# Kernel tuning notes

Measured on AMD Instinct MI355X. Metric: run time of the kernel, lower is better.

The kernel has to match this reference:

```python
import jax, jax.numpy as jnp
import numpy as np

B, M, PAST, FUT, NPRED, D = 512, 32768, 8, 12, 20, 48


def _gru_step(h, x, w_ih, w_hh, b_ih, b_hh):
    # torch GRU cell: gates ordered [r, z, n]
    gi = x @ w_ih.T + b_ih
    gh = h @ w_hh.T + b_hh
    ir, iz, inn = jnp.split(gi, 3, axis=-1)
    hr, hz, hn = jnp.split(gh, 3, axis=-1)
    r = jax.nn.sigmoid(ir + hr)
    z = jax.nn.sigmoid(iz + hz)
    n = jnp.tanh(inn + r * hn)
    return (1.0 - z) * n + z * h


def setup_inputs() -> dict:
    key = jax.random.key(0)
    ks = jax.random.split(key, 16)
    f32 = jnp.float32
    def rn(k, shp, sc):
        return (jax.random.normal(k, shp, dtype=f32) * sc)
    return {
        "past": jax.random.normal(ks[0], (B, PAST, 2), dtype=f32),
        "obs_traj": jax.random.normal(ks[1], (B, PAST, 2), dtype=f32),
        "conv_w": rn(ks[2], (D, 2, 3), 0.3),
        "conv_b": jnp.zeros((D,), f32),
        "enc_w_ih": rn(ks[3], (3 * D, D), 0.1),
        "enc_w_hh": rn(ks[4], (3 * D, D), 0.1),
        "enc_b_ih": jnp.zeros((3 * D,), f32),
        "enc_b_hh": jnp.zeros((3 * D,), f32),
        "memory_past": jax.random.normal(ks[5], (M, D), dtype=f32),
        "memory_fut": jax.random.normal(ks[6], (M, D), dtype=f32),
        "Wq": rn(ks[7], (D, D), 0.1), "bq": jnp.zeros((D,), f32),
        "Wk": rn(ks[8], (D, D), 0.1), "bk": jnp.zeros((D,), f32),
        "Wv": rn(ks[9], (D, D), 0.1), "bv": jnp.zeros((D,), f32),
        "dec_w_ih": rn(ks[10], (6 * D, 2 * D), 0.1),
        "dec_w_hh": rn(ks[11], (6 * D, 2 * D), 0.1),
        "dec_b_ih": jnp.zeros((6 * D,), f32),
        "dec_b_hh": jnp.zeros((6 * D,), f32),
        "fc_w": rn(ks[12], (2, 2 * D), 0.1),
        "fc_b": jnp.zeros((2,), f32),
    }


def reference(past, obs_traj, conv_w, conv_b, enc_w_ih, enc_w_hh, enc_b_ih, enc_b_hh,
              memory_past, memory_fut, Wq, bq, Wk, bk, Wv, bv,
              dec_w_ih, dec_w_hh, dec_b_ih, dec_b_hh, fc_w, fc_b):
    b = past.shape[0]
    # --- past encoder: Conv1d(2,48,3,pad=1) + ReLU, then GRU(48,48) ---
    x = jnp.transpose(past, (0, 2, 1))                     # [B,2,T]
    emb = jax.lax.conv_general_dilated(
        x, conv_w, (1,), [(1, 1)], dimension_numbers=("NCH", "OIH", "NCH"))
    emb = jax.nn.relu(emb + conv_b[None, :, None])         # [B,48,T]
    emb = jnp.transpose(emb, (2, 0, 1))                    # [T,B,48] for scan

    def enc_step(h, x_t):
        return _gru_step(h, x_t, enc_w_ih, enc_w_hh, enc_b_ih, enc_b_hh), None
    state_past, _ = jax.lax.scan(enc_step, jnp.zeros((b, D), past.dtype), emb)  # [B,48]

    # --- iterative refinement: 20 rounds of attention over the full memory ---
    # Lin_K/Lin_V are applied to the same (full) banks every iteration -> hoist.
    K = memory_past @ Wk.T + bk                            # [M,48]
    V = memory_fut @ Wv.T + bv                             # [M,48]

    def irm_step(c, _):
        q = c @ Wq.T + bq                                  # [B,48]
        a = jax.nn.softmax(q @ K.T, axis=-1)               # [B,M], scale=1.0
        att = a @ V                                        # [B,48]
        return q + att, att
    _, atts = jax.lax.scan(irm_step, state_past, None, length=NPRED)  # [20,B,48]
    pred = jnp.transpose(atts, (1, 0, 2)).reshape(-1, D)   # [B*20,48] (b-major)

    # --- GRU(96,96) decoder, future_len steps, input only at t=0 ---
    n = b * NPRED
    present = jnp.repeat(obs_traj[:, -1], NPRED, axis=0)   # [B*20,2]
    sp = jnp.repeat(state_past, NPRED, axis=0)             # [B*20,48]
    info = jnp.concatenate([sp, pred], axis=1)             # [B*20,96]
    xs = jnp.concatenate(
        [info[None], jnp.zeros((FUT - 1, n, 2 * D), info.dtype)], axis=0)

    def dec_step(carry, x_t):
        h, pres = carry
        h = _gru_step(h, x_t, dec_w_ih, dec_w_hh, dec_b_ih, dec_b_hh)
        pres = pres + (h @ fc_w.T + fc_b)
        return (h, pres), pres
    _, coords = jax.lax.scan(
        dec_step, (jnp.zeros((n, 2 * D), info.dtype), present), xs)  # [FUT,B*20,2]

    prediction = jnp.transpose(coords, (1, 0, 2)).reshape(b, NPRED, FUT, 2)
    return prediction
```

## Files before the change

### kernel.cpp

```cpp
#include <hip/hip_runtime.h>

typedef unsigned short u16;
typedef unsigned int u32;
typedef __attribute__((ext_vector_type(8))) short short8v;
typedef __attribute__((ext_vector_type(4))) float f32x4;

#define GLD_LDS(g, l) __builtin_amdgcn_global_load_lds( \
    (const __attribute__((address_space(1))) void*)(g), \
    (__attribute__((address_space(3))) void*)(l), 16, 0, 0)

#define LOG2E 1.44269504f

__device__ __forceinline__ u16 f2bf(float f){
  union { float f; u32 u; } v; v.f = f;
  u32 r = v.u + 0x7FFFu + ((v.u >> 16) & 1u);
  return (u16)(r >> 16);
}
__device__ __forceinline__ float bf2f(u16 h){
  union { u32 u; float f; } v; v.u = ((u32)h) << 16;
  return v.f;
}
__device__ __forceinline__ u32 pk2(float a, float b){
  union { float f; u32 u; } x, y; x.f = a; y.f = b;
  return __builtin_amdgcn_perm(y.u + 0x8000u, x.u + 0x8000u, 0x07060302u);
}
__device__ __forceinline__ float sigm(float x){ return 1.f/(1.f+__expf(-x)); }
__device__ __forceinline__ float tanh_fast(float x){ return 1.f - 2.f/(1.f+__expf(2.f*x)); }

__global__ __launch_bounds__(256) void setup_kernel(
    const float* past, const float* conv_w, const float* conv_b,
    const float* enc_w_ih, const float* enc_w_hh, const float* enc_b_ih, const float* enc_b_hh,
    const float* memory_past, const float* memory_fut,
    const float* Wq, const float* bq, const float* Wk, const float* bk,
    const float* Wv, const float* bv,
    const float* dec_w_ih, const float* dec_w_hh,
    float* stateP, float* qf, u16* qbB,
    u16* Kb, u16* Vc, u16* Dihf, u16* Dhhf, u16* WqF)
{
  __shared__ __align__(16) char SMEM[61440];
  const int tid = threadIdx.x, bx = blockIdx.x;
  const int wid = tid>>6, lane = tid&63, qd = lane>>4, ln = lane&15;
  f32x4 zf = {0.f,0.f,0.f,0.f};

  if (tid < 108){
    int which = (tid >= 54) ? 1 : 0;
    int e = bx*54 + (tid - which*54);
    const float* src = which ? dec_w_hh : dec_w_ih;
    u16* dst = which ? Dhhf : Dihf;
    int j = e&7, l2 = (e>>3)&15, q2 = (e>>7)&3, tkc = e>>9;
    int kc = tkc % 3, nt = tkc / 3;
    dst[e] = f2bf(src[(nt*16+l2)*96 + kc*32 + q2*8 + j]);
  }
  if (bx < 12){
    int e = bx*256 + tid;
    int j = e&7, l2 = (e>>3)&15, q2 = (e>>7)&3, tkc = e>>9;
    int kc = tkc&1, nt = tkc>>1;
    int g = nt*16+l2, k = kc*32+q2*8+j;
    WqF[e] = (k < 48) ? f2bf(Wq[g*48+k]) : (u16)0;
  }

  if (bx >= 504){
    int eb = bx - 504;
    u16* sWih = (u16*)(SMEM);
    u16* sWhh = (u16*)(SMEM + 18432);
    u16* sWq  = (u16*)(SMEM + 36864);
    float* sCw = (float*)(SMEM + 43008);
    float* sCb = (float*)(SMEM + 44160);
    float* sPast = (float*)(SMEM + 44352);
    u16* sHbW = (u16*)(SMEM + 48448 + wid*2304);
    for (int e0 = tid; e0 < 21504; e0 += 256){
      int e = e0; const float* src; u16* dst;
      if (e < 9216){ src = enc_w_ih; dst = sWih; }
      else if (e < 18432){ e -= 9216; src = enc_w_hh; dst = sWhh; }
      else { e -= 18432; src = Wq; dst = sWq; }
      int j = e&7, l2 = (e>>3)&15, q2 = (e>>7)&3, tkc = e>>9;
      int kc = tkc&1, nt = tkc>>1;
      int g = nt*16+l2, k = kc*32+q2*8+j;
      dst[e] = (k < 48) ? f2bf(src[g*48+k]) : (u16)0;
    }
    for (int i = tid; i < 288; i += 256) sCw[i] = conv_w[i];
    if (tid < 48) sCb[tid] = conv_b[tid];
    for (int i = tid; i < 1024; i += 256) sPast[i] = past[eb*1024 + i];
    __syncthreads();
    short8v aE[8][2];
    {
      const float* pr = &sPast[(wid*16 + ln)*16];
      for (int t = 0; t < 8; ++t)
        for (int kc = 0; kc < 2; ++kc){
          union { short8v v; u16 h[8]; } u;
          #pragma unroll
          for (int j = 0; j < 8; ++j){
            int d = kc*32 + qd*8 + j;
            float a = 0.f;
            if (d < 48){
              a = sCb[d];
              #pragma unroll
              for (int kt = 0; kt < 3; ++kt){
                int tau = t + kt - 1;
                if (tau >= 0 && tau < 8){
                  a += pr[tau*2+0]*sCw[d*6+kt];
                  a += pr[tau*2+1]*sCw[d*6+3+kt];
                }
              }
              a = fmaxf(a, 0.f);
            }
            u.h[j] = (d < 48) ? f2bf(a) : (u16)0;
          }
          aE[t][kc] = u.v;
        }
    }
    for (int i = lane; i < 576; i += 64) ((u32*)sHbW)[i] = 0;
    float biR[3],biZ[3],biN[3],bhR[3],bhZ[3],bhN[3];
    #pragma unroll
    for (int i = 0; i < 3; ++i){
      int d = i*16 + ln;
      biR[i]=enc_b_ih[d]; biZ[i]=enc_b_ih[48+d]; biN[i]=enc_b_ih[96+d];
      bhR[i]=enc_b_hh[d]; bhZ[i]=enc_b_hh[48+d]; bhN[i]=enc_b_hh[96+d];
    }
    float hreg[3][4];
    #pragma unroll
    for (int i=0;i<3;++i) for (int r=0;r<4;++r) hreg[i][r]=0.f;
    int r0 = eb*64 + wid*16;
    #pragma unroll 1
    for (int t = 0; t < 8; ++t){
      short8v aH0 = *(const short8v*)&sHbW[ln*72 + qd*8];
      short8v aH1 = *(const short8v*)&sHbW[ln*72 + 32 + qd*8];
      f32x4 gI[9], gH[9];
      #pragma unroll
      for (int nt = 0; nt < 9; ++nt){ gI[nt] = zf; gH[nt] = zf; }
      #pragma unroll
      for (int nt = 0; nt < 9; ++nt){
        gI[nt] = __builtin_amdgcn_mfma_f32_16x16x32_bf16(aE[t][0], *(const short8v*)&sWih[((nt*2+0)*4+qd)*128 + ln*8], gI[nt], 0,0,0);
        gI[nt] = __builtin_amdgcn_mfma_f32_16x16x32_bf16(aE[t][1], *(const short8v*)&sWih[((nt*2+1)*4+qd)*128 + ln*8], gI[nt], 0,0,0);
        gH[nt] = __builtin_amdgcn_mfma_f32_16x16x32_bf16(aH0, *(const short8v*)&sWhh[((nt*2+0)*4+qd)*128 + ln*8], gH[nt], 0,0,0);
        gH[nt] = __builtin_amdgcn_mfma_f32_16x16x32_bf16(aH1, *(const short8v*)&sWhh[((nt*2+1)*4+qd)*128 + ln*8], gH[nt], 0,0,0);
      }
      #pragma unroll
      for (int i3 = 0; i3 < 3; ++i3)
        #pragma unroll
        for (int r = 0; r < 4; ++r){
          float rr = sigm(gI[i3][r]+biR[i3] + gH[i3][r]+bhR[i3]);
          float zz = sigm(gI[i3+3][r]+biZ[i3] + gH[i3+3][r]+bhZ[i3]);
          float nn = tanh_fast(gI[i3+6][r]+biN[i3] + rr*(gH[i3+6][r]+bhN[i3]));
          float hv = (1.f-zz)*nn + zz*hreg[i3][r];
          hreg[i3][r] = hv;
          sHbW[(qd*4+r)*72 + i3*16 + ln] = f2bf(hv);
        }
    }
    #pragma unroll
    for (int i3 = 0; i3 < 3; ++i3)
      #pragma unroll
      for (int r = 0; r < 4; ++r)
        stateP[(r0+qd*4+r)*48 + i3*16 + ln] = hreg[i3][r];
    short8v aH0 = *(const short8v*)&sHbW[ln*72 + qd*8];
    short8v aH1 = *(const short8v*)&sHbW[ln*72 + 32 + qd*8];
    f32x4 q3[3];
    #pragma unroll
    for (int nt = 0; nt < 3; ++nt){
      q3[nt] = zf;
      q3[nt] = __builtin_amdgcn_mfma_f32_16x16x32_bf16(aH0, *(const short8v*)&sWq[((nt*2+0)*4+qd)*128 + ln*8], q3[nt], 0,0,0);
      q3[nt] = __builtin_amdgcn_mfma_f32_16x16x32_bf16(aH1, *(const short8v*)&sWq[((nt*2+1)*4+qd)*128 + ln*8], q3[nt], 0,0,0);
    }
    #pragma unroll
    for (int nt = 0; nt < 3; ++nt)
      #pragma unroll
      for (int r = 0; r < 4; ++r){
        int row = r0 + qd*4 + r, d = nt*16 + ln;
        float v = q3[nt][r] + bq[d];
        qf[row*48 + d] = v;
        qbB[row*64 + d] = f2bf(v * LOG2E);
      }
    #pragma unroll
    for (int r = 0; r < 4; ++r)
      if (ln < 8) *(u32*)&qbB[(r0+qd*4+r)*64 + 48 + ln*2] = 0;
  } else {
    u16* sWkF = (u16*)(SMEM);
    u16* sWvF = (u16*)(SMEM + 6144);
    u16* smp  = (u16*)(SMEM + 12288 + wid*2304);
    u16* smf  = (u16*)(SMEM + 21504 + wid*2304);
    for (int e0 = tid; e0 < 6144; e0 += 256){
      int e = e0; const float* src; u16* dst;
      if (e < 3072){ src = Wk; dst = sWkF; } else { e -= 3072; src = Wv; dst = sWvF; }
      int j = e&7, l2 = (e>>3)&15, q2 = (e>>7)&3, tkc = e>>9;
      int kc = tkc&1, nt = tkc>>1;
      int g = nt*16+l2, k = kc*32+q2*8+j;
      dst[e] = (k < 48) ? f2bf(src[g*48+k]) : (u16)0;
    }
    __syncthreads();
    int ntile = (bx < 8) ? 2 : 1;
    for (int tt = 0; tt < ntile; ++tt){
      int tile = (tt == 0) ? bx : (504 + bx);
      int r0 = tile*64 + wid*16;
      for (int i = lane; i < 576; i += 64){ ((u32*)smp)[i] = 0; ((u32*)smf)[i] = 0; }
      for (int i = lane; i < 768; i += 64){
        int r = i/48, c = i - r*48;
        smp[r*72+c] = f2bf(memory_past[(size_t)r0*48 + i]);
        smf[r*72+c] = f2bf(memory_fut[(size_t)r0*48 + i]);
      }
      short8v aP0 = *(const short8v*)&smp[ln*72 + qd*8];
      short8v aP1 = *(const short8v*)&smp[ln*72 + 32 + qd*8];
      short8v aF0 = *(const short8v*)&smf[ln*72 + qd*8];
      short8v aF1 = *(const short8v*)&smf[ln*72 + 32 + qd*8];
      f32x4 k3[3], v3[3];
      #pragma unroll
      for (int nt = 0; nt < 3; ++nt){ k3[nt] = zf; v3[nt] = zf; }
      #pragma unroll
      for (int nt = 0; nt < 3; ++nt){
        k3[nt] = __builtin_amdgcn_mfma_f32_16x16x32_bf16(aP0, *(const short8v*)&sWkF[((nt*2+0)*4+qd)*128 + ln*8], k3[nt], 0,0,0);
        k3[nt] = __builtin_amdgcn_mfma_f32_16x16x32_bf16(aP1, *(const short8v*)&sWkF[((nt*2+1)*4+qd)*128 + ln*8], k3[nt], 0,0,0);
        v3[nt] = __builtin_amdgcn_mfma_f32_16x16x32_bf16(aF0, *(const short8v*)&sWvF[((nt*2+0)*4+qd)*128 + ln*8], v3[nt], 0,0,0);
        v3[nt] = __builtin_amdgcn_mfma_f32_16x16x32_bf16(aF1, *(const short8v*)&sWvF[((nt*2+1)*4+qd)*128 + ln*8], v3[nt], 0,0,0);
      }
      #pragma unroll
      for (int nt = 0; nt < 3; ++nt)
        #pragma unroll
        for (int r = 0; r < 4; ++r){
          int key = r0 + qd*4 + r, d = nt*16 + ln;
          Kb[(size_t)key*64 + d] = f2bf(k3[nt][r] + bk[d]);
          Vc[((size_t)(key>>8)*48 + d)*256 + (key&255)] = f2bf(v3[nt][r] + bv[d]);
        }
      #pragma unroll
      for (int r = 0; r < 4; ++r)
        if (ln < 8){ int key = r0 + qd*4 + r; *(u32*)&Kb[(size_t)key*64 + 48 + ln*2] = 0; }
    }
  }
}

__global__ __launch_bounds__(256) void iter_kernel(int mode, int it,
    const u16* qbB, const u16* Kb, const u16* Vc, const u16* WqF, const float* bq,
    const float* qfP, float* qfC, float* pred,
    const float* mP, const float* lP, const float* aP,
    float* mC, float* lC, float* aC)
{
  __shared__ __align__(16) u16 sQ[32*64];
  __shared__ __align__(16) u16 sp8[8][16*72];
  __shared__ float sMg[4][32*50];
  __shared__ float sWc[32*16];
  __shared__ float sLg[32];
  __shared__ __align__(16) u16 sCb[32*72];
  const int tid = threadIdx.x, bx = blockIdx.x;
  const int wid = tid>>6, lane = tid&63, qd = lane>>4, ln = lane&15;
  f32x4 zf = {0.f,0.f,0.f,0.f};

  if (mode == 2){
    int lrow = tid>>4, j = tid&15;
    int row = bx*16 + lrow;
    float m = mP[row*16 + j], l = lP[row*16 + j];
    float mg = m;
    #pragma unroll
    for (int k = 1; k < 16; k <<= 1) mg = fmaxf(mg, __shfl_xor(mg, k));
    float w = exp2f(m - mg);
    float wl = w*l;
    #pragma unroll
    for (int k = 1; k < 16; k <<= 1) wl += __shfl_xor(wl, k);
    sWc[lrow*16 + j] = w;
    if (j == 0) sLg[lrow] = wl;
    __syncthreads();
    float lg = sLg[lrow];
    #pragma unroll
    for (int k2 = 0; k2 < 3; ++k2){
      int d = j + k2*16;
      float a = 0.f;
      #pragma unroll 4
      for (int c = 0; c < 16; ++c) a += sWc[lrow*16+c]*aP[(size_t)(row*16+c)*48 + d];
      pred[(size_t)(row*20 + 19)*48 + d] = a / lg;
    }
    return;
  }

  const int rg = bx>>4, ch = bx&15;
  const int rowbase = rg*32;

  if (mode == 1){
    int row = tid>>3, jj = tid&7, grow = rowbase + row;
    float m0 = mP[grow*16 + jj*2], m1 = mP[grow*16 + jj*2+1];
    float l0 = lP[grow*16 + jj*2], l1 = lP[grow*16 + jj*2+1];
    float mg = fmaxf(m0, m1);
    #pragma unroll
    for (int k = 1; k < 8; k <<= 1) mg = fmaxf(mg, __shfl_xor(mg, k));
    float w0 = exp2f(m0 - mg), w1 = exp2f(m1 - mg);
    float wl = w0*l0 + w1*l1;
    #pragma unroll
    for (int k = 1; k < 8; k <<= 1) wl += __shfl_xor(wl, k);
    sWc[row*16 + jj*2] = w0; sWc[row*16 + jj*2+1] = w1;
    if (jj == 0) sLg[row] = wl;
    __syncthreads();
    float lg = sLg[row];
    int d0 = jj*6;
    float aa[6] = {0,0,0,0,0,0};
    #pragma unroll 4
    for (int c = 0; c < 16; ++c){
      float w = sWc[row*16 + c];
      const float* ap = aP + (size_t)(grow*16 + c)*48 + d0;
      #pragma unroll
      for (int d6 = 0; d6 < 6; ++d6) aa[d6] += w*ap[d6];
    }
    #pragma unroll
    for (int d6 = 0; d6 < 6; ++d6){
      int d = d0 + d6;
      float a = aa[d6] / lg;
      if (ch == 0) pred[(size_t)(grow*20 + (it-1))*48 + d] = a;
      sCb[row*72 + d] = f2bf(qfP[grow*48 + d] + a);
    }
    { int r2 = tid>>3, p = tid&7; ((u32*)&sCb[r2*72 + 48])[p] = 0; }
    __syncthreads();
    if (wid < 2){
      short8v ac0 = *(const short8v*)&sCb[(wid*16+ln)*72 + qd*8];
      short8v ac1 = *(const short8v*)&sCb[(wid*16+ln)*72 + 32 + qd*8];
      f32x4 q3[3];
      #pragma unroll
      for (int nt = 0; nt < 3; ++nt){
        q3[nt] = zf;
        q3[nt] = __builtin_amdgcn_mfma_f32_16x16x32_bf16(ac0, *(const short8v*)&WqF[((nt*2+0)*4+qd)*128 + ln*8], q3[nt], 0,0,0);
        q3[nt] = __builtin_amdgcn_mfma_f32_16x16x32_bf16(ac1, *(const short8v*)&WqF[((nt*2+1)*4+qd)*128 + ln*8], q3[nt], 0,0,0);
      }
      #pragma unroll
      for (int nt = 0; nt < 3; ++nt)
        #pragma unroll
        for (int r = 0; r < 4; ++r){
          int lr = wid*16 + qd*4 + r, d = nt*16 + ln;
          float v = q3[nt][r] + bq[d];
          if (ch == 0) qfC[(rowbase + lr)*48 + d] = v;
          sQ[lr*64 + d] = f2bf(v * LOG2E);
        }
    } else {
      for (int i = tid-128; i < 256; i += 128){
        int r2 = i>>3, p = i&7;
        ((u32*)&sQ[r2*64 + 48])[p] = 0;
      }
    }
    __syncthreads();
  } else {
    const u32* src = (const u32*)(qbB + rowbase*64);
    ((u32*)sQ)[tid]       = src[tid];
    ((u32*)sQ)[256 + tid] = src[256 + tid];
    ((u32*)sQ)[512 + tid] = src[512 + tid];
    ((u32*)sQ)[768 + tid] = src[768 + tid];
    __syncthreads();
  }

  const int wslice = ch*2048 + wid*512;
  short8v aq[2][2];
  #pragma unroll
  for (int rt = 0; rt < 2; ++rt)
    #pragma unroll
    for (int kc = 0; kc < 2; ++kc)
      aq[rt][kc] = *(const short8v*)&sQ[(rt*16+ln)*64 + kc*32 + qd*8];
  f32x4 acc[2][3];
  #pragma unroll
  for (int rt = 0; rt < 2; ++rt) for (int dt = 0; dt < 3; ++dt) acc[rt][dt] = zf;
  float mrun[2] = {-3.0e38f, -3.0e38f}, lrun[2] = {0.f, 0.f};
  u16* spb[2] = { sp8[wid*2], sp8[wid*2+1] };

  #pragma unroll
  for (int kt = 0; kt < 8; ++kt){
    const int tb = wslice + kt*64;
    const u16* kb = Kb + (size_t)tb*64;
    const u16* vb = Vc + (size_t)(tb>>8)*48*256 + (tb & 255);
    short8v kf[4][2], vf[2][3];
    #pragma unroll
    for (int nt = 0; nt < 4; ++nt)
      #pragma unroll
      for (int kc = 0; kc < 2; ++kc)
        kf[nt][kc] = *(const short8v*)&kb[(nt*16+ln)*64 + kc*32 + qd*8];
    #pragma unroll
    for (int kc = 0; kc < 2; ++kc)
      #pragma unroll
      for (int dt = 0; dt < 3; ++dt)
        vf[kc][dt] = *(const short8v*)&vb[(dt*16+ln)*256 + kc*32 + qd*8];
    f32x4 s[2][4];
    #pragma unroll
    for (int rt = 0; rt < 2; ++rt)
      #pragma unroll
      for (int nt = 0; nt < 4; ++nt){
        f32x4 z = zf;
        z = __builtin_amdgcn_mfma_f32_16x16x32_bf16(kf[nt][0], aq[rt][0], z, 0,0,0);
        z = __builtin_amdgcn_mfma_f32_16x16x32_bf16(kf[nt][1], aq[rt][1], z, 0,0,0);
        s[rt][nt] = z;
      }
    #pragma unroll
    for (int rt = 0; rt < 2; ++rt){
      float vmax = fmaxf(fmaxf(fmaxf(s[rt][0][0], s[rt][0][1]), fmaxf(s[rt][0][2], s[rt][0][3])),
                   fmaxf(fmaxf(s[rt][1][0], s[rt][1][1]), fmaxf(s[rt][1][2], s[rt][1][3])));
      vmax = fmaxf(vmax, fmaxf(fmaxf(fmaxf(s[rt][2][0], s[rt][2][1]), fmaxf(s[rt][2][2], s[rt][2][3])),
                   fmaxf(fmaxf(s[rt][3][0], s[rt][3][1]), fmaxf(s[rt][3][2], s[rt][3][3]))));
      vmax = fmaxf(vmax, __shfl_xor(vmax, 16));
      vmax = fmaxf(vmax, __shfl_xor(vmax, 32));
      float mnew = fmaxf(mrun[rt], vmax);
      float alpha = exp2f(mrun[rt] - mnew);
      mrun[rt] = mnew;
      u16* sp = spb[rt];
      float lsum = 0.f;
      #pragma unroll
      for (int nt = 0; nt < 4; ++nt){
        float p0 = exp2f(s[rt][nt][0]-mnew), p1 = exp2f(s[rt][nt][1]-mnew);
        float p2 = exp2f(s[rt][nt][2]-mnew), p3 = exp2f(s[rt][nt][3]-mnew);
        lsum += (p0+p1)+(p2+p3);
        uint2 pk; pk.x = pk2(p0,p1); pk.y = pk2(p2,p3);
        *(uint2*)&sp[ln*72 + nt*16 + qd*4] = pk;
      }
      lsum += __shfl_xor(lsum, 16);
      lsum += __shfl_xor(lsum, 32);
      lrun[rt] = lrun[rt]*alpha + lsum;
      #pragma unroll
      for (int dt = 0; dt < 3; ++dt){
        acc[rt][dt][0] *= alpha; acc[rt][dt][1] *= alpha;
        acc[rt][dt][2] *= alpha; acc[rt][dt][3] *= alpha;
      }
      short8v pb0 = *(const short8v*)&sp[ln*72 + qd*8];
      short8v pb1 = *(const short8v*)&sp[ln*72 + 32 + qd*8];
      #pragma unroll
      for (int dt = 0; dt < 3; ++dt){
        acc[rt][dt] = __builtin_amdgcn_mfma_f32_16x16x32_bf16(vf[0][dt], pb0, acc[rt][dt], 0,0,0);
        acc[rt][dt] = __builtin_amdgcn_mfma_f32_16x16x32_bf16(vf[1][dt], pb1, acc[rt][dt], 0,0,0);
      }
    }
  }
  #pragma unroll
  for (int rt = 0; rt < 2; ++rt)
    #pragma unroll
    for (int dt = 0; dt < 3; ++dt)
      #pragma unroll
      for (int r = 0; r < 4; ++r)
        sMg[wid][(rt*16+ln)*50 + dt*16 + qd*4 + r] = acc[rt][dt][r];
  if (lane < 16){
    sMg[wid][ln*50 + 48] = mrun[0]; sMg[wid][ln*50 + 49] = lrun[0];
    sMg[wid][(16+ln)*50 + 48] = mrun[1]; sMg[wid][(16+ln)*50 + 49] = lrun[1];
  }
  __syncthreads();
  {
    int row = tid>>3, jj = tid&7, grow = rowbase + row;
    float m0 = sMg[0][row*50+48], m1 = sMg[1][row*50+48];
    float m2 = sMg[2][row*50+48], m3 = sMg[3][row*50+48];
    float mg = fmaxf(fmaxf(m0,m1), fmaxf(m2,m3));
    float e0 = exp2f(m0-mg), e1 = exp2f(m1-mg), e2 = exp2f(m2-mg), e3 = exp2f(m3-mg);
    float lg = e0*sMg[0][row*50+49] + e1*sMg[1][row*50+49]
             + e2*sMg[2][row*50+49] + e3*sMg[3][row*50+49];
    if (jj == 0){ mC[grow*16 + ch] = mg; lC[grow*16 + ch] = lg; }
    int d0 = jj*6;
    #pragma unroll
    for (int d6 = 0; d6 < 6; ++d6){
      int d = d0 + d6;
      aC[(size_t)(grow*16 + ch)*48 + d] =
          e0*sMg[0][row*50+d] + e1*sMg[1][row*50+d]
        + e2*sMg[2][row*50+d] + e3*sMg[3][row*50+d];
    }
  }
}

__global__ __launch_bounds__(128) void dec_kernel(
    const u16* Dihf, const u16* Dhhf, const float* b_ih, const float* b_hh,
    const float* stateP, const float* pred, const float* obs,
    const float* fc_w, const float* fc_b, float* out)
{
  __shared__ __align__(16) u16 sW[27648];
  __shared__ __align__(16) u16 sX[2][16*104];
  const int tid = threadIdx.x, bx = blockIdx.x;
  const int wid = tid>>6, lane = tid&63, qd = lane>>4, ln = lane&15;
  f32x4 zf = {0.f,0.f,0.f,0.f};
  for (int i = wid; i < 54; i += 2)
    GLD_LDS((const char*)Dihf + i*1024 + lane*16, (char*)sW + i*1024);
  u16* sx = sX[wid];
  int rw = (bx*2 + wid)*16;
  for (int i = lane; i < 1536; i += 64){
    int r = i/96, k = i - r*96;
    int row = rw + r, b20 = row/20;
    float v = (k < 48) ? stateP[b20*48 + k] : pred[(size_t)row*48 + (k-48)];
    sx[r*104 + k] = f2bf(v);
  }
  float fw0[6], fw1[6];
  float biR[6],biZ[6],biN[6],bhR[6],bhZ[6],bhN[6];
  #pragma unroll
  for (int i = 0; i < 6; ++i){
    int d = i*16 + ln;
    fw0[i] = fc_w[d]; fw1[i] = fc_w[96+d];
    biR[i]=b_ih[d]; biZ[i]=b_ih[96+d]; biN[i]=b_ih[192+d];
    bhR[i]=b_hh[d]; bhZ[i]=b_hh[96+d]; bhN[i]=b_hh[192+d];
  }
  float fcb0 = fc_b[0], fcb1 = fc_b[1];
  float pr0[4], pr1[4];
  #pragma unroll
  for (int r = 0; r < 4; ++r){
    int b20 = (rw + qd*4 + r)/20;
    pr0[r] = obs[b20*16 + 14];
    pr1[r] = obs[b20*16 + 15];
  }
  __syncthreads();
  #pragma unroll 1
  for (int t = 0; t < 12; ++t){
    if (t == 1){
      __syncthreads();
      for (int i = wid; i < 54; i += 2)
        GLD_LDS((const char*)Dhhf + i*1024 + lane*16, (char*)sW + i*1024);
      __syncthreads();
    }
    short8v xa0 = *(const short8v*)&sx[ln*104 + qd*8];
    short8v xa1 = *(const short8v*)&sx[ln*104 + 32 + qd*8];
    short8v xa2 = *(const short8v*)&sx[ln*104 + 64 + qd*8];
    f32x4 acc[18];
    #pragma unroll
    for (int i = 0; i < 18; ++i) acc[i] = zf;
    #pragma unroll
    for (int nt = 0; nt < 18; ++nt){
      acc[nt] = __builtin_amdgcn_mfma_f32_16x16x32_bf16(xa0, *(const short8v*)&sW[((nt*3+0)*4+qd)*128 + ln*8], acc[nt], 0,0,0);
      acc[nt] = __builtin_amdgcn_mfma_f32_16x16x32_bf16(xa1, *(const short8v*)&sW[((nt*3+1)*4+qd)*128 + ln*8], acc[nt], 0,0,0);
      acc[nt] = __builtin_amdgcn_mfma_f32_16x16x32_bf16(xa2, *(const short8v*)&sW[((nt*3+2)*4+qd)*128 + ln*8], acc[nt], 0,0,0);
    }
    float px[4] = {0,0,0,0}, py[4] = {0,0,0,0};
    #pragma unroll
    for (int r = 0; r < 4; ++r)
      #pragma unroll
      for (int i = 0; i < 6; ++i){
        int d = i*16 + ln;
        float rr = sigm(acc[i][r]   + biR[i] + bhR[i]);
        float zz = sigm(acc[i+6][r] + biZ[i] + bhZ[i]);
        float nn, hold;
        if (t == 0){
          nn = tanh_fast(acc[i+12][r] + biN[i] + rr*bhN[i]);
          hold = 0.f;
        } else {
          nn = tanh_fast(biN[i] + rr*(acc[i+12][r] + bhN[i]));
          hold = bf2f(sx[(qd*4+r)*104 + d]);
        }
        float hv = (1.f-zz)*nn + zz*hold;
        sx[(qd*4+r)*104 + d] = f2bf(hv);
        px[r] += fw0[i]*hv;
        py[r] += fw1[i]*hv;
      }
    #pragma unroll
    for (int msk = 8; msk >= 1; msk >>= 1)
      #pragma unroll
      for (int r = 0; r < 4; ++r){
        px[r] += __shfl_xor(px[r], msk);
        py[r] += __shfl_xor(py[r], msk);
      }
    #pragma unroll
    for (int r = 0; r < 4; ++r){
      pr0[r] += px[r] + fcb0;
      pr1[r] += py[r] + fcb1;
    }
    if (ln == 0){
      #pragma unroll
      for (int r = 0; r < 4; ++r){
        int row = rw + qd*4 + r;
        out[(size_t)(row*12 + t)*2 + 0] = pr0[r];
        out[(size_t)(row*12 + t)*2 + 1] = pr1[r];
      }
    }
  }
}

extern "C" void kernel_launch(void* const* d_in, const int* in_sizes, int n_in,
                              void* d_out, int out_size, void* d_ws, size_t ws_size,
                              hipStream_t stream)
{
  const float* past        = (const float*)d_in[0];
  const float* obs         = (const float*)d_in[1];
  const float* conv_w      = (const float*)d_in[2];
  const float* conv_b      = (const float*)d_in[3];
  const float* enc_w_ih    = (const float*)d_in[4];
  const float* enc_w_hh    = (const float*)d_in[5];
  const float* enc_b_ih    = (const float*)d_in[6];
  const float* enc_b_hh    = (const float*)d_in[7];
  const float* memory_past = (const float*)d_in[8];
  const float* memory_fut  = (const float*)d_in[9];
  const float* Wq = (const float*)d_in[10];
  const float* bq = (const float*)d_in[11];
  const float* Wk = (const float*)d_in[12];
  const float* bk = (const float*)d_in[13];
  const float* Wv = (const float*)d_in[14];
  const float* bv = (const float*)d_in[15];
  const float* dec_w_ih = (const float*)d_in[16];
  const float* dec_w_hh = (const float*)d_in[17];
  const float* dec_b_ih = (const float*)d_in[18];
  const float* dec_b_hh = (const float*)d_in[19];
  const float* fc_w = (const float*)d_in[20];
  const float* fc_b = (const float*)d_in[21];
  float* out = (float*)d_out;

  char* ws = (char*)d_ws;
  size_t off = 0;
  auto alloc = [&](size_t bytes){ void* p = ws + off; off += (bytes + 255) & ~(size_t)255; return p; };
  float* stateP = (float*)alloc(512*48*4);
  float* qfA    = (float*)alloc(512*48*4);
  float* qfB    = (float*)alloc(512*48*4);
  u16*   qbB    = (u16*)alloc(512*64*2);
  float* mB[2], *lB[2], *aB[2];
  for (int i = 0; i < 2; ++i){
    mB[i] = (float*)alloc(512*16*4);
    lB[i] = (float*)alloc(512*16*4);
    aB[i] = (float*)alloc((size_t)512*16*48*4);
  }
  float* pred = (float*)alloc((size_t)10240*48*4);
  u16*   Kb   = (u16*)alloc((size_t)32768*64*2);
  u16*   Vc   = (u16*)alloc((size_t)32768*48*2);
  u16*   Dihf = (u16*)alloc(27648*2);
  u16*   Dhhf = (u16*)alloc(27648*2);
  u16*   WqF  = (u16*)alloc(3072*2);
  float* qbuf[2] = { qfA, qfB };

  setup_kernel<<<512, 256, 0, stream>>>(
      past, conv_w, conv_b, enc_w_ih, enc_w_hh, enc_b_ih, enc_b_hh,
      memory_past, memory_fut, Wq, bq, Wk, bk, Wv, bv, dec_w_ih, dec_w_hh,
      stateP, qfA, qbB, Kb, Vc, Dihf, Dhhf, WqF);

  iter_kernel<<<256, 256, 0, stream>>>(0, 0, qbB, Kb, Vc, WqF, bq,
      qfA, qfA, pred, mB[1], lB[1], aB[1], mB[0], lB[0], aB[0]);
  for (int it = 1; it < 20; ++it){
    int pv = (it-1)&1, cu = it&1;
    iter_kernel<<<256, 256, 0, stream>>>(1, it, qbB, Kb, Vc, WqF, bq,
        qbuf[pv], qbuf[cu], pred, mB[pv], lB[pv], aB[pv], mB[cu], lB[cu], aB[cu]);
  }
  iter_kernel<<<32, 256, 0, stream>>>(2, 20, qbB, Kb, Vc, WqF, bq,
      qbuf[1], qbuf[0], pred, mB[1], lB[1], aB[1], mB[0], lB[0], aB[0]);

  dec_kernel<<<320, 128, 0, stream>>>(Dihf, Dhhf, dec_b_ih, dec_b_hh,
      stateP, pred, obs, fc_w, fc_b, out);
}
```

Baseline: 658.9 us.

## Fuse final softmax merge into decoder, prefetch first K/V tile, alias shared memory

The final attention-merge launch is removed and its work folded into the decoder kernel, which now uses 64-thread blocks (640 of them), reads the input-projection weights for step 0 directly from global memory, and loads the recurrent weights into LDS once up front. The iteration kernel hoists the first K/V tile load above the merge/query stage so it overlaps that work. It aliases its shared buffers into one block to shrink LDS and stores partial attention outputs in a chunk-major layout. The partial merge now runs as a coalesced vectorised reduction across waves. The cost is more serial work per decoder block and extra register pressure from the prefetched fragments.

```diff
diff --git a/kernel.cpp b/kernel.cpp
--- a/kernel.cpp
+++ b/kernel.cpp
@@ -232,77 +232,88 @@
     const float* mP, const float* lP, const float* aP,
     float* mC, float* lC, float* aC)
 {
-  __shared__ __align__(16) u16 sQ[32*64];
-  __shared__ __align__(16) u16 sp8[8][16*72];
-  __shared__ float sMg[4][32*50];
-  __shared__ float sWc[32*16];
-  __shared__ float sLg[32];
-  __shared__ __align__(16) u16 sCb[32*72];
+  __shared__ __align__(16) char SMEM[55936];
+  u16*   sQ  = (u16*)(SMEM + 45056);
+  float* sWc = (float*)(SMEM + 49152);
+  float* sLg = (float*)(SMEM + 51200);
+  u16*   sCb = (u16*)(SMEM + 51332);
   const int tid = threadIdx.x, bx = blockIdx.x;
   const int wid = tid>>6, lane = tid&63, qd = lane>>4, ln = lane&15;
-  f32x4 zf = {0.f,0.f,0.f,0.f};
-
-  if (mode == 2){
-    int lrow = tid>>4, j = tid&15;
-    int row = bx*16 + lrow;
-    float m = mP[row*16 + j], l = lP[row*16 + j];
-    float mg = m;
-    #pragma unroll
-    for (int k = 1; k < 16; k <<= 1) mg = fmaxf(mg, __shfl_xor(mg, k));
-    float w = exp2f(m - mg);
-    float wl = w*l;
-    #pragma unroll
-    for (int k = 1; k < 16; k <<= 1) wl += __shfl_xor(wl, k);
-    sWc[lrow*16 + j] = w;
-    if (j == 0) sLg[lrow] = wl;
-    __syncthreads();
-    float lg = sLg[lrow];
-    #pragma unroll
-    for (int k2 = 0; k2 < 3; ++k2){
-      int d = j + k2*16;
-      float a = 0.f;
-      #pragma unroll 4
-      for (int c = 0; c < 16; ++c) a += sWc[lrow*16+c]*aP[(size_t)(row*16+c)*48 + d];
-      pred[(size_t)(row*20 + 19)*48 + d] = a / lg;
-    }
-    return;
-  }
-
   const int rg = bx>>4, ch = bx&15;
   const int rowbase = rg*32;
+  f32x4 zf = {0.f,0.f,0.f,0.f};
+
+  const int wslice = ch*2048 + wid*512;
+  short8v kf0[4][2], vf0[2][3];
+  {
+    const u16* kb = Kb + (size_t)wslice*64;
+    const u16* vb = Vc + (size_t)(wslice>>8)*48*256 + (wslice & 255);
+    #pragma unroll
+    for (int nt = 0; nt < 4; ++nt)
+      #pragma unroll
+      for (int kc = 0; kc < 2; ++kc)
+        kf0[nt][kc] = *(const short8v*)&kb[(nt*16+ln)*64 + kc*32 + qd*8];
+    #pragma unroll
+    for (int kc = 0; kc < 2; ++kc)
+      #pragma unroll
+      for (int dt = 0; dt < 3; ++dt)
+        vf0[kc][dt] = *(const short8v*)&vb[(dt*16+ln)*256 + kc*32 + qd*8];
+  }
 
   if (mode == 1){
-    int row = tid>>3, jj = tid&7, grow = rowbase + row;
-    float m0 = mP[grow*16 + jj*2], m1 = mP[grow*16 + jj*2+1];
-    float l0 = lP[grow*16 + jj*2], l1 = lP[grow*16 + jj*2+1];
-    float mg = fmaxf(m0, m1);
-    #pragma unroll
-    for (int k = 1; k < 8; k <<= 1) mg = fmaxf(mg, __shfl_xor(mg, k));
-    float w0 = exp2f(m0 - mg), w1 = exp2f(m1 - mg);
-    float wl = w0*l0 + w1*l1;
-    #pragma unroll
-    for (int k = 1; k < 8; k <<= 1) wl += __shfl_xor(wl, k);
-    sWc[row*16 + jj*2] = w0; sWc[row*16 + jj*2+1] = w1;
-    if (jj == 0) sLg[row] = wl;
+    float* sRed = (float*)SMEM;
+    {
+      int row = tid>>3, jj = tid&7, grow = rowbase + row;
+      float m0 = mP[grow*16 + jj*2], m1 = mP[grow*16 + jj*2+1];
+      float l0 = lP[grow*16 + jj*2], l1 = lP[grow*16 + jj*2+1];
+      float mg = fmaxf(m0, m1);
+      #pragma unroll
+      for (int k = 1; k < 8; k <<= 1) mg = fmaxf(mg, __shfl_xor(mg, k));
+      float w0 = exp2f(m0 - mg), w1 = exp2f(m1 - mg);
+      float wl = w0*l0 + w1*l1;
+      #pragma unroll
+      for (int k = 1; k < 8; k <<= 1) wl += __shfl_xor(wl, k);
+      sWc[row*16 + jj*2] = w0; sWc[row*16 + jj*2+1] = w1;
+      if (jj == 0) sLg[row] = wl;
+    }
     __syncthreads();
-    float lg = sLg[row];
-    int d0 = jj*6;
-    float aa[6] = {0,0,0,0,0,0};
-    #pragma unroll 4
-    for (int c = 0; c < 16; ++c){
-      float w = sWc[row*16 + c];
-      const float* ap = aP + (size_t)(grow*16 + c)*48 + d0;
-      #pragma unroll
-      for (int d6 = 0; d6 < 6; ++d6) aa[d6] += w*ap[d6];
-    }
-    #pragma unroll
-    for (int d6 = 0; d6 < 6; ++d6){
-      int d = d0 + d6;
-      float a = aa[d6] / lg;
-      if (ch == 0) pred[(size_t)(grow*20 + (it-1))*48 + d] = a;
-      sCb[row*72 + d] = f2bf(qfP[grow*48 + d] + a);
-    }
-    { int r2 = tid>>3, p = tid&7; ((u32*)&sCb[r2*72 + 48])[p] = 0; }
+    {
+      f32x4 accv[6];
+      #pragma unroll
+      for (int i = 0; i < 6; ++i) accv[i] = zf;
+      #pragma unroll
+      for (int ci = 0; ci < 4; ++ci){
+        int c = wid*4 + ci;
+        const f32x4* slab = (const f32x4*)(aP + ((size_t)c*512 + rowbase)*48);
+        #pragma unroll
+        for (int i = 0; i < 6; ++i){
+          f32x4 v = slab[i*64 + lane];
+          int rr = (i*64 + lane)/12;
+          float w = sWc[rr*16 + c];
+          accv[i][0] += w*v[0]; accv[i][1] += w*v[1];
+          accv[i][2] += w*v[2]; accv[i][3] += w*v[3];
+        }
+      }
+      float* red = sRed + wid*1536;
+      #pragma unroll
+      for (int i = 0; i < 6; ++i)
+        *(f32x4*)&red[(i*64 + lane)*4] = accv[i];
+    }
+    __syncthreads();
+    {
+      int row = tid>>3, jj = tid&7, grow = rowbase + row;
+      float lg = sLg[row];
+      int base = row*48 + jj*6;
+      #pragma unroll
+      for (int d6 = 0; d6 < 6; ++d6){
+        int d = jj*6 + d6;
+        float s = sRed[base+d6] + sRed[1536+base+d6] + sRed[3072+base+d6] + sRed[4608+base+d6];
+        float a = s / lg;
+        if (ch == 0) pred[(size_t)(grow*20 + (it-1))*48 + d] = a;
+        sCb[row*72 + d] = f2bf(qfP[grow*48 + d] + a);
+      }
+      ((u32*)&sCb[row*72 + 48])[jj] = 0;
+    }
     __syncthreads();
     if (wid < 2){
       short8v ac0 = *(const short8v*)&sCb[(wid*16+ln)*72 + qd*8];
@@ -339,7 +350,7 @@
     __syncthreads();
   }
 
-  const int wslice = ch*2048 + wid*512;
+  u16* sp8 = (u16*)(SMEM + 26624);
   short8v aq[2][2];
   #pragma unroll
   for (int rt = 0; rt < 2; ++rt)
@@ -350,7 +361,7 @@
   #pragma unroll
   for (int rt = 0; rt < 2; ++rt) for (int dt = 0; dt < 3; ++dt) acc[rt][dt] = zf;
   float mrun[2] = {-3.0e38f, -3.0e38f}, lrun[2] = {0.f, 0.f};
-  u16* spb[2] = { sp8[wid*2], sp8[wid*2+1] };
+  u16* spb[2] = { sp8 + (wid*2+0)*1152, sp8 + (wid*2+1)*1152 };
 
   #pragma unroll
   for (int kt = 0; kt < 8; ++kt){
@@ -358,16 +369,27 @@
     const u16* kb = Kb + (size_t)tb*64;
     const u16* vb = Vc + (size_t)(tb>>8)*48*256 + (tb & 255);
     short8v kf[4][2], vf[2][3];
-    #pragma unroll
-    for (int nt = 0; nt < 4; ++nt)
+    if (kt == 0){
+      #pragma unroll
+      for (int nt = 0; nt < 4; ++nt)
+        #pragma unroll
+        for (int kc = 0; kc < 2; ++kc) kf[nt][kc] = kf0[nt][kc];
       #pragma unroll
       for (int kc = 0; kc < 2; ++kc)
-        kf[nt][kc] = *(const short8v*)&kb[(nt*16+ln)*64 + kc*32 + qd*8];
-    #pragma unroll
-    for (int kc = 0; kc < 2; ++kc)
-      #pragma unroll
-      for (int dt = 0; dt < 3; ++dt)
-        vf[kc][dt] = *(const short8v*)&vb[(dt*16+ln)*256 + kc*32 + qd*8];
+        #pragma unroll
+        for (int dt = 0; dt < 3; ++dt) vf[kc][dt] = vf0[kc][dt];
+    } else {
+      #pragma unroll
+      for (int nt = 0; nt < 4; ++nt)
+        #pragma unroll
+        for (int kc = 0; kc < 2; ++kc)
+          kf[nt][kc] = *(const short8v*)&kb[(nt*16+ln)*64 + kc*32 + qd*8];
+      #pragma unroll
+      for (int kc = 0; kc < 2; ++kc)
+        #pragma unroll
+        for (int dt = 0; dt < 3; ++dt)
+          vf[kc][dt] = *(const short8v*)&vb[(dt*16+ln)*256 + kc*32 + qd*8];
+    }
     f32x4 s[2][4];
     #pragma unroll
     for (int rt = 0; rt < 2; ++rt)
@@ -416,58 +438,83 @@
       }
     }
   }
+  __syncthreads();
+  float* sMg = (float*)SMEM;
   #pragma unroll
   for (int rt = 0; rt < 2; ++rt)
     #pragma unroll
     for (int dt = 0; dt < 3; ++dt)
       #pragma unroll
       for (int r = 0; r < 4; ++r)
-        sMg[wid][(rt*16+ln)*50 + dt*16 + qd*4 + r] = acc[rt][dt][r];
+        sMg[wid*1600 + (rt*16+ln)*50 + dt*16 + qd*4 + r] = acc[rt][dt][r];
   if (lane < 16){
-    sMg[wid][ln*50 + 48] = mrun[0]; sMg[wid][ln*50 + 49] = lrun[0];
-    sMg[wid][(16+ln)*50 + 48] = mrun[1]; sMg[wid][(16+ln)*50 + 49] = lrun[1];
+    sMg[wid*1600 + ln*50 + 48] = mrun[0]; sMg[wid*1600 + ln*50 + 49] = lrun[0];
+    sMg[wid*1600 + (16+ln)*50 + 48] = mrun[1]; sMg[wid*1600 + (16+ln)*50 + 49] = lrun[1];
   }
   __syncthreads();
   {
     int row = tid>>3, jj = tid&7, grow = rowbase + row;
-    float m0 = sMg[0][row*50+48], m1 = sMg[1][row*50+48];
-    float m2 = sMg[2][row*50+48], m3 = sMg[3][row*50+48];
+    float m0 = sMg[row*50+48], m1 = sMg[1600+row*50+48];
+    float m2 = sMg[3200+row*50+48], m3 = sMg[4800+row*50+48];
     float mg = fmaxf(fmaxf(m0,m1), fmaxf(m2,m3));
     float e0 = exp2f(m0-mg), e1 = exp2f(m1-mg), e2 = exp2f(m2-mg), e3 = exp2f(m3-mg);
-    float lg = e0*sMg[0][row*50+49] + e1*sMg[1][row*50+49]
-             + e2*sMg[2][row*50+49] + e3*sMg[3][row*50+49];
+    float lg = e0*sMg[row*50+49] + e1*sMg[1600+row*50+49]
+             + e2*sMg[3200+row*50+49] + e3*sMg[4800+row*50+49];
     if (jj == 0){ mC[grow*16 + ch] = mg; lC[grow*16 + ch] = lg; }
     int d0 = jj*6;
     #pragma unroll
     for (int d6 = 0; d6 < 6; ++d6){
       int d = d0 + d6;
-      aC[(size_t)(grow*16 + ch)*48 + d] =
-          e0*sMg[0][row*50+d] + e1*sMg[1][row*50+d]
-        + e2*sMg[2][row*50+d] + e3*sMg[3][row*50+d];
+      aC[((size_t)ch*512 + grow)*48 + d] =
+          e0*sMg[row*50+d] + e1*sMg[1600+row*50+d]
+        + e2*sMg[3200+row*50+d] + e3*sMg[4800+row*50+d];
     }
   }
 }
 
-__global__ __launch_bounds__(128) void dec_kernel(
+__global__ __launch_bounds__(64) void dec_kernel(
     const u16* Dihf, const u16* Dhhf, const float* b_ih, const float* b_hh,
     const float* stateP, const float* pred, const float* obs,
+    const float* mF, const float* lF, const float* aF,
     const float* fc_w, const float* fc_b, float* out)
 {
   __shared__ __align__(16) u16 sW[27648];
-  __shared__ __align__(16) u16 sX[2][16*104];
-  const int tid = threadIdx.x, bx = blockIdx.x;
-  const int wid = tid>>6, lane = tid&63, qd = lane>>4, ln = lane&15;
+  __shared__ __align__(16) u16 sx[16*104];
+  const int lane = threadIdx.x, bx = blockIdx.x;
+  const int qd = lane>>4, ln = lane&15;
   f32x4 zf = {0.f,0.f,0.f,0.f};
-  for (int i = wid; i < 54; i += 2)
-    GLD_LDS((const char*)Dihf + i*1024 + lane*16, (char*)sW + i*1024);
-  u16* sx = sX[wid];
-  int rw = (bx*2 + wid)*16;
+  const int rw = bx*16;
+
+  #pragma unroll 1
+  for (int i = 0; i < 54; ++i)
+    GLD_LDS((const char*)Dhhf + i*1024 + lane*16, (char*)sW + i*1024);
+
   for (int i = lane; i < 1536; i += 64){
     int r = i/96, k = i - r*96;
     int row = rw + r, b20 = row/20;
     float v = (k < 48) ? stateP[b20*48 + k] : pred[(size_t)row*48 + (k-48)];
     sx[r*104 + k] = f2bf(v);
   }
+  {
+    int r19 = (19 - (rw % 20)) % 20;
+    if (r19 < 16 && lane < 48){
+      int b = (rw + r19)/20;
+      float mg = -3.0e38f;
+      float mv[16];
+      #pragma unroll
+      for (int c = 0; c < 16; ++c){ mv[c] = mF[b*16 + c]; mg = fmaxf(mg, mv[c]); }
+      float num = 0.f, den = 0.f;
+      #pragma unroll
+      for (int c = 0; c < 16; ++c){
+        float w = exp2f(mv[c] - mg);
+        den += w * lF[b*16 + c];
+        num += w * aF[((size_t)c*512 + b)*48 + lane];
+      }
+      sx[r19*104 + 48 + lane] = f2bf(num/den);
+    }
+  }
+  __syncthreads();
+
   float fw0[6], fw1[6];
   float biR[6],biZ[6],biN[6],bhR[6],bhZ[6],bhN[6];
   #pragma unroll
@@ -485,15 +532,8 @@
     pr0[r] = obs[b20*16 + 14];
     pr1[r] = obs[b20*16 + 15];
   }
-  __syncthreads();
-  #pragma unroll 1
-  for (int t = 0; t < 12; ++t){
-    if (t == 1){
-      __syncthreads();
-      for (int i = wid; i < 54; i += 2)
-        GLD_LDS((const char*)Dhhf + i*1024 + lane*16, (char*)sW + i*1024);
-      __syncthreads();
-    }
+
+  {
     short8v xa0 = *(const short8v*)&sx[ln*104 + qd*8];
     short8v xa1 = *(const short8v*)&sx[ln*104 + 32 + qd*8];
     short8v xa2 = *(const short8v*)&sx[ln*104 + 64 + qd*8];
@@ -502,9 +542,9 @@
     for (int i = 0; i < 18; ++i) acc[i] = zf;
     #pragma unroll
     for (int nt = 0; nt < 18; ++nt){
-      acc[nt] = __builtin_amdgcn_mfma_f32_16x16x32_bf16(xa0, *(const short8v*)&sW[((nt*3+0)*4+qd)*128 + ln*8], acc[nt], 0,0,0);
-      acc[nt] = __builtin_amdgcn_mfma_f32_16x16x32_bf16(xa1, *(const short8v*)&sW[((nt*3+1)*4+qd)*128 + ln*8], acc[nt], 0,0,0);
-      acc[nt] = __builtin_amdgcn_mfma_f32_16x16x32_bf16(xa2, *(const short8v*)&sW[((nt*3+2)*4+qd)*128 + ln*8], acc[nt], 0,0,0);
+      acc[nt] = __builtin_amdgcn_mfma_f32_16x16x32_bf16(xa0, *(const short8v*)&Dihf[((nt*3+0)*4+qd)*128 + ln*8], acc[nt], 0,0,0);
+      acc[nt] = __builtin_amdgcn_mfma_f32_16x16x32_bf16(xa1, *(const short8v*)&Dihf[((nt*3+1)*4+qd)*128 + ln*8], acc[nt], 0,0,0);
+      acc[nt] = __builtin_amdgcn_mfma_f32_16x16x32_bf16(xa2, *(const short8v*)&Dihf[((nt*3+2)*4+qd)*128 + ln*8], acc[nt], 0,0,0);
     }
     float px[4] = {0,0,0,0}, py[4] = {0,0,0,0};
     #pragma unroll
@@ -514,14 +554,59 @@
         int d = i*16 + ln;
         float rr = sigm(acc[i][r]   + biR[i] + bhR[i]);
         float zz = sigm(acc[i+6][r] + biZ[i] + bhZ[i]);
-        float nn, hold;
-        if (t == 0){
-          nn = tanh_fast(acc[i+12][r] + biN[i] + rr*bhN[i]);
-          hold = 0.f;
-        } else {
-          nn = tanh_fast(biN[i] + rr*(acc[i+12][r] + bhN[i]));
-          hold = bf2f(sx[(qd*4+r)*104 + d]);
-        }
+        float nn = tanh_fast(acc[i+12][r] + biN[i] + rr*bhN[i]);
+        float hv = (1.f-zz)*nn;
+        sx[(qd*4+r)*104 + d] = f2bf(hv);
+        px[r] += fw0[i]*hv;
+        py[r] += fw1[i]*hv;
+      }
+    #pragma unroll
+    for (int msk = 8; msk >= 1; msk >>= 1)
+      #pragma unroll
+      for (int r = 0; r < 4; ++r){
+        px[r] += __shfl_xor(px[r], msk);
+        py[r] += __shfl_xor(py[r], msk);
+      }
+    #pragma unroll
+    for (int r = 0; r < 4; ++r){
+      pr0[r] += px[r] + fcb0;
+      pr1[r] += py[r] + fcb1;
+    }
+    if (ln == 0){
+      #pragma unroll
+      for (int r = 0; r < 4; ++r){
+        int row = rw + qd*4 + r;
+        out[(size_t)(row*12 + 0)*2 + 0] = pr0[r];
+        out[(size_t)(row*12 + 0)*2 + 1] = pr1[r];
+      }
+    }
+  }
+  __syncthreads();
+
+  #pragma unroll 1
+  for (int t = 1; t < 12; ++t){
+    short8v xa0 = *(const short8v*)&sx[ln*104 + qd*8];
+    short8v xa1 = *(const short8v*)&sx[ln*104 + 32 + qd*8];
+    short8v xa2 = *(const short8v*)&sx[ln*104 + 64 + qd*8];
+    f32x4 acc[18];
+    #pragma unroll
+    for (int i = 0; i < 18; ++i) acc[i] = zf;
+    #pragma unroll
+    for (int nt = 0; nt < 18; ++nt){
+      acc[nt] = __builtin_amdgcn_mfma_f32_16x16x32_bf16(xa0, *(const short8v*)&sW[((nt*3+0)*4+qd)*128 + ln*8], acc[nt], 0,0,0);
+      acc[nt] = __builtin_amdgcn_mfma_f32_16x16x32_bf16(xa1, *(const short8v*)&sW[((nt*3+1)*4+qd)*128 + ln*8], acc[nt], 0,0,0);
+      acc[nt] = __builtin_amdgcn_mfma_f32_16x16x32_bf16(xa2, *(const short8v*)&sW[((nt*3+2)*4+qd)*128 + ln*8], acc[nt], 0,0,0);
+    }
+    float px[4] = {0,0,0,0}, py[4] = {0,0,0,0};
+    #pragma unroll
+    for (int r = 0; r < 4; ++r)
+      #pragma unroll
+      for (int i = 0; i < 6; ++i){
+        int d = i*16 + ln;
+        float rr = sigm(acc[i][r]   + biR[i] + bhR[i]);
+        float zz = sigm(acc[i+6][r] + biZ[i] + bhZ[i]);
+        float nn = tanh_fast(biN[i] + rr*(acc[i+12][r] + bhN[i]));
+        float hold = bf2f(sx[(qd*4+r)*104 + d]);
         float hv = (1.f-zz)*nn + zz*hold;
         sx[(qd*4+r)*104 + d] = f2bf(hv);
         px[r] += fw0[i]*hv;
@@ -611,9 +696,7 @@
     iter_kernel<<<256, 256, 0, stream>>>(1, it, qbB, Kb, Vc, WqF, bq,
         qbuf[pv], qbuf[cu], pred, mB[pv], lB[pv], aB[pv], mB[cu], lB[cu], aB[cu]);
   }
-  iter_kernel<<<32, 256, 0, stream>>>(2, 20, qbB, Kb, Vc, WqF, bq,
-      qbuf[1], qbuf[0], pred, mB[1], lB[1], aB[1], mB[0], lB[0], aB[0]);
-
-  dec_kernel<<<320, 128, 0, stream>>>(Dihf, Dhhf, dec_b_ih, dec_b_hh,
-      stateP, pred, obs, fc_w, fc_b, out);
+
+  dec_kernel<<<640, 64, 0, stream>>>(Dihf, Dhhf, dec_b_ih, dec_b_hh,
+      stateP, pred, obs, mB[1], lB[1], aB[1], fc_w, fc_b, out);
 }
```

Result: slower. 719.0 us (+9.1%).
